# Optimization experiments

Hardware: AMD Instinct MI355X
Metric: run time of the kernel (lower is better)

## Reference

```python
import jax, jax.numpy as jnp
import numpy as np

B, S, IN, OUT, RANK, LORA_R = 2, 2048, 4096, 4096, 8, 16
LORA_SCALING = 16.0 / LORA_R  # alpha / r = 1.0


def setup_inputs() -> dict:
    key = jax.random.key(0)
    ks = jax.random.split(key, 6)
    x = jax.random.normal(ks[0], (B, S, IN), dtype=jnp.float32)
    weight = jax.random.normal(ks[1], (OUT, IN), dtype=jnp.float32) * 0.02  # Q (snapped weights)
    scale_A = jax.random.normal(ks[2], (OUT, RANK), dtype=jnp.float32) * 0.1
    scale_B = jax.random.normal(ks[3], (RANK, IN), dtype=jnp.float32) * 0.1
    rank_magnitude = jnp.ones((RANK,), dtype=jnp.float32)
    lora_A = jax.random.normal(ks[4], (LORA_R, IN), dtype=jnp.float32) * 0.02
    lora_B = jax.random.normal(ks[5], (OUT, LORA_R), dtype=jnp.float32) * 0.02
    return {"x": x, "weight": weight, "scale_A": scale_A, "scale_B": scale_B,
            "rank_magnitude": rank_magnitude, "lora_A": lora_A, "lora_B": lora_B}


def reference(x, weight, scale_A, scale_B, rank_magnitude, lora_A, lora_B):
    # y_o = sum_k g_k * a_{ok} * sum_i Q_{oi} * b_{ki} * x_i
    #     = sum_i (Q_{oi} * sum_k (g_k a_{ok}) b_{ki}) x_i
    # i.e. a single dense GEMM with the precomputed effective weight
    # W_eff = Q * ((scale_A * g) @ scale_B)  -- same math, rank dim folded once.
    S_mat = jnp.einsum('ok,ki->oi', scale_A * rank_magnitude[None, :], scale_B)  # [out, in]
    W_eff = weight * S_mat                                                        # [out, in]
    y = jnp.einsum('bsi,oi->bso', x, W_eff)                                       # [B, S, out]
    # LoRA add: (x @ A^T) @ B^T * scaling
    y = y + ((x @ lora_A.T) @ lora_B.T) * LORA_SCALING
    return y
```

## Files before the change

kernel.cpp:

```cpp
#include <hip/hip_runtime.h>

#define M_DIM 4096
#define IN_DIM 4096
#define OUT_DIM 4096
#define RANK 8
#define LORA_R 16
#define LORA_SCALING 1.0f

typedef __bf16 bf16;
typedef bf16  bf16x4 __attribute__((ext_vector_type(4)));
typedef bf16  bf16x8 __attribute__((ext_vector_type(8)));
typedef float f32x4  __attribute__((ext_vector_type(4)));
typedef float f32x16 __attribute__((ext_vector_type(16)));

#define OG 8
__global__ __launch_bounds__(256) void prep_weight(
    const float* __restrict__ weight, const float* __restrict__ scale_A,
    const float* __restrict__ scale_B, const float* __restrict__ g,
    const float* __restrict__ lora_A, const float* __restrict__ lora_B,
    bf16* __restrict__ wt)
{
    __shared__ float s_sa[OG][RANK];
    __shared__ float s_lb[OG][LORA_R];
    const int o0 = blockIdx.x * OG;
    const int t  = threadIdx.x;
    if (t < OG * RANK) {
        int r8 = t / RANK, k = t % RANK;
        s_sa[r8][k] = scale_A[(o0 + r8) * RANK + k] * g[k];
    }
    if (t < OG * LORA_R) {
        int r8 = t / LORA_R, r = t % LORA_R;
        s_lb[r8][r] = lora_B[(o0 + r8) * LORA_R + r] * LORA_SCALING;
    }
    __syncthreads();

    const int i0 = (blockIdx.y * 256 + t) * 4;

    f32x4 acc[OG];
#pragma unroll
    for (int r8 = 0; r8 < OG; ++r8) acc[r8] = {0.f, 0.f, 0.f, 0.f};
#pragma unroll
    for (int k = 0; k < RANK; ++k) {
        f32x4 sbk = *(const f32x4*)(scale_B + k * IN_DIM + i0);
#pragma unroll
        for (int r8 = 0; r8 < OG; ++r8) acc[r8] += s_sa[r8][k] * sbk;
    }
#pragma unroll
    for (int r8 = 0; r8 < OG; ++r8) {
        f32x4 wv = *(const f32x4*)(weight + (size_t)(o0 + r8) * IN_DIM + i0);
        acc[r8] *= wv;
    }
#pragma unroll
    for (int r = 0; r < LORA_R; ++r) {
        f32x4 lak = *(const f32x4*)(lora_A + r * IN_DIM + i0);
#pragma unroll
        for (int r8 = 0; r8 < OG; ++r8) acc[r8] += s_lb[r8][r] * lak;
    }
#pragma unroll
    for (int r8 = 0; r8 < OG; ++r8) {
        bf16x4 h = { (bf16)acc[r8][0], (bf16)acc[r8][1],
                     (bf16)acc[r8][2], (bf16)acc[r8][3] };
        *(bf16x4*)(wt + (size_t)(o0 + r8) * IN_DIM + i0) = h;
    }
}

__global__ __launch_bounds__(256) void cast_x(
    const float* __restrict__ x, bf16* __restrict__ xb, int n4)
{
    int idx    = blockIdx.x * blockDim.x + threadIdx.x;
    int stride = gridDim.x * blockDim.x;
    for (int i = idx; i < n4; i += stride) {
        f32x4 v = *(const f32x4*)(x + (size_t)i * 4);
        bf16x4 h = { (bf16)v[0], (bf16)v[1], (bf16)v[2], (bf16)v[3] };
        *(bf16x4*)(xb + (size_t)i * 4) = h;
    }
}

#define BM 128
#define BN 128
#define BK 32

__device__ __forceinline__ void gload_lds16(const bf16* g, bf16* l) {
    __builtin_amdgcn_global_load_lds(
        (const __attribute__((address_space(1))) void*)g,
        (__attribute__((address_space(3))) void*)l,
        16, 0, 0);
}

__global__ __launch_bounds__(256) void gemm_bt(
    const bf16* __restrict__ A,
    const bf16* __restrict__ Bw,
    float* __restrict__ C)
{
    __shared__ __align__(16) char smem[16896];
    bf16* sA = (bf16*)smem;
    bf16* sB = (bf16*)(smem + 8192);

    const int t    = threadIdx.x;
    const int w    = t >> 6;
    const int lane = t & 63;
    const int lh   = lane >> 5;
    const int ln   = lane & 31;

    const int bid = blockIdx.x;
    const int xcd = bid & 7;
    const int rr_ = bid >> 3;
    const int m0  = (xcd * 4 + (rr_ & 3)) * BM;
    const int n0  = (rr_ >> 2) * BN;

    const int wm = (w >> 1) * 64;
    const int wn = (w & 1) * 64;

    const int srow = t >> 2;
    const int scol = ((t & 3) ^ (srow & 3)) * 8;
    const bf16* gA0 = A  + (size_t)(m0 + srow)      * IN_DIM + scol;
    const bf16* gA1 = A  + (size_t)(m0 + 64 + srow) * IN_DIM + scol;
    const bf16* gB0 = Bw + (size_t)(n0 + srow)      * IN_DIM + scol;
    const bf16* gB1 = Bw + (size_t)(n0 + 64 + srow) * IN_DIM + scol;
    bf16* lA0 = sA + w * 512;
    bf16* lA1 = sA + 2048 + w * 512;
    bf16* lB0 = sB + w * 512;
    bf16* lB1 = sB + 2048 + w * 512;

    const bf16* pA[2][2];
    const bf16* pB[2][2];
#pragma unroll
    for (int tm = 0; tm < 2; ++tm) {
        int rowA = wm + tm * 32 + ln;
        int rowB = wn + tm * 32 + ln;
#pragma unroll
        for (int s = 0; s < 2; ++s) {
            pA[tm][s] = sA + rowA * 32 + (((s * 2 + lh) ^ (rowA & 3)) * 8);
            pB[tm][s] = sB + rowB * 32 + (((s * 2 + lh) ^ (rowB & 3)) * 8);
        }
    }

    f32x16 acc[2][2] = {};

    for (int k0 = 0; k0 < IN_DIM; k0 += BK) {
        __syncthreads();
        gload_lds16(gA0 + k0, lA0);
        gload_lds16(gA1 + k0, lA1);
        gload_lds16(gB0 + k0, lB0);
        gload_lds16(gB1 + k0, lB1);
        __syncthreads();

        bf16x8 af[2][2], bf_[2][2];
#pragma unroll
        for (int tm = 0; tm < 2; ++tm)
#pragma unroll
            for (int s = 0; s < 2; ++s) {
                af[tm][s]  = *(const bf16x8*)pA[tm][s];
                bf_[tm][s] = *(const bf16x8*)pB[tm][s];
            }
#pragma unroll
        for (int s = 0; s < 2; ++s)
#pragma unroll
            for (int tm = 0; tm < 2; ++tm)
#pragma unroll
                for (int tn = 0; tn < 2; ++tn)
                    acc[tm][tn] = __builtin_amdgcn_mfma_f32_32x32x16_bf16(
                        af[tm][s], bf_[tn][s], acc[tm][tn], 0, 0, 0);
    }

    __syncthreads();
    float* sEw = (float*)smem + w * (32 * 33);
#pragma unroll
    for (int tm = 0; tm < 2; ++tm)
#pragma unroll
        for (int tn = 0; tn < 2; ++tn) {
#pragma unroll
            for (int j = 0; j < 16; ++j) {
                int row = (j & 3) + 8 * (j >> 2) + 4 * lh;
                sEw[row * 33 + ln] = acc[tm][tn][j];
            }
#pragma unroll
            for (int p = 0; p < 4; ++p) {
                int r4 = p * 8 + (lane >> 3);
                int c4 = (lane & 7) * 4;
                f32x4 v = { sEw[r4 * 33 + c4],     sEw[r4 * 33 + c4 + 1],
                            sEw[r4 * 33 + c4 + 2], sEw[r4 * 33 + c4 + 3] };
                *(f32x4*)(C + (size_t)(m0 + wm + tm * 32 + r4) * OUT_DIM
                            + (n0 + wn + tn * 32 + c4)) = v;
            }
        }
}

extern "C" void kernel_launch(void* const* d_in, const int* in_sizes, int n_in,
                              void* d_out, int out_size, void* d_ws, size_t ws_size,
                              hipStream_t stream) {
    (void)in_sizes; (void)n_in; (void)out_size; (void)ws_size;
    const float* x        = (const float*)d_in[0];
    const float* weight   = (const float*)d_in[1];
    const float* scale_A  = (const float*)d_in[2];
    const float* scale_B  = (const float*)d_in[3];
    const float* g        = (const float*)d_in[4];
    const float* lora_A   = (const float*)d_in[5];
    const float* lora_B   = (const float*)d_in[6];
    float* out = (float*)d_out;

    bf16* xb = (bf16*)d_ws;
    bf16* wt = (bf16*)((char*)d_ws + (size_t)M_DIM * IN_DIM * sizeof(bf16));

    dim3 pgrid(OUT_DIM / OG, IN_DIM / (256 * 4));
    prep_weight<<<pgrid, 256, 0, stream>>>(weight, scale_A, scale_B, g,
                                           lora_A, lora_B, wt);
    cast_x<<<2048, 256, 0, stream>>>(x, xb, (M_DIM * IN_DIM) / 4);

    gemm_bt<<<(M_DIM / BM) * (OUT_DIM / BN), 256, 0, stream>>>(xb, wt, out);
}
```

Baseline: 360.4 us.

## Fuse weight prep and x cast into one launch; change LDS swizzle pattern

Merges the weight-prep and x-cast kernels into a single launch, with the first 2048 blocks building the effective bf16 weight and the rest casting x. This removes one kernel launch and lets both memory-bound passes run concurrently. The GEMM's LDS XOR swizzle now keys on (row>>1)&3 instead of row&3, to cut bank conflicts on the MFMA fragment reads. The load-side and read-side swizzles must stay consistent; the load side uses (t>>3)&3, which equals (srow>>1)&3.

```diff
diff --git a/kernel.cpp b/kernel.cpp
--- a/kernel.cpp
+++ b/kernel.cpp
@@ -14,65 +14,64 @@
 typedef float f32x16 __attribute__((ext_vector_type(16)));
 
 #define OG 8
-__global__ __launch_bounds__(256) void prep_weight(
+__global__ __launch_bounds__(256) void prep_fused(
     const float* __restrict__ weight, const float* __restrict__ scale_A,
     const float* __restrict__ scale_B, const float* __restrict__ g,
     const float* __restrict__ lora_A, const float* __restrict__ lora_B,
-    bf16* __restrict__ wt)
+    const float* __restrict__ x, bf16* __restrict__ wt, bf16* __restrict__ xb)
 {
-    __shared__ float s_sa[OG][RANK];
-    __shared__ float s_lb[OG][LORA_R];
-    const int o0 = blockIdx.x * OG;
-    const int t  = threadIdx.x;
-    if (t < OG * RANK) {
-        int r8 = t / RANK, k = t % RANK;
-        s_sa[r8][k] = scale_A[(o0 + r8) * RANK + k] * g[k];
-    }
-    if (t < OG * LORA_R) {
-        int r8 = t / LORA_R, r = t % LORA_R;
-        s_lb[r8][r] = lora_B[(o0 + r8) * LORA_R + r] * LORA_SCALING;
-    }
-    __syncthreads();
-
-    const int i0 = (blockIdx.y * 256 + t) * 4;
-
-    f32x4 acc[OG];
-#pragma unroll
-    for (int r8 = 0; r8 < OG; ++r8) acc[r8] = {0.f, 0.f, 0.f, 0.f};
-#pragma unroll
-    for (int k = 0; k < RANK; ++k) {
-        f32x4 sbk = *(const f32x4*)(scale_B + k * IN_DIM + i0);
-#pragma unroll
-        for (int r8 = 0; r8 < OG; ++r8) acc[r8] += s_sa[r8][k] * sbk;
-    }
-#pragma unroll
-    for (int r8 = 0; r8 < OG; ++r8) {
-        f32x4 wv = *(const f32x4*)(weight + (size_t)(o0 + r8) * IN_DIM + i0);
-        acc[r8] *= wv;
-    }
-#pragma unroll
-    for (int r = 0; r < LORA_R; ++r) {
-        f32x4 lak = *(const f32x4*)(lora_A + r * IN_DIM + i0);
-#pragma unroll
-        for (int r8 = 0; r8 < OG; ++r8) acc[r8] += s_lb[r8][r] * lak;
-    }
-#pragma unroll
-    for (int r8 = 0; r8 < OG; ++r8) {
-        bf16x4 h = { (bf16)acc[r8][0], (bf16)acc[r8][1],
-                     (bf16)acc[r8][2], (bf16)acc[r8][3] };
-        *(bf16x4*)(wt + (size_t)(o0 + r8) * IN_DIM + i0) = h;
-    }
-}
-
-__global__ __launch_bounds__(256) void cast_x(
-    const float* __restrict__ x, bf16* __restrict__ xb, int n4)
-{
-    int idx    = blockIdx.x * blockDim.x + threadIdx.x;
-    int stride = gridDim.x * blockDim.x;
-    for (int i = idx; i < n4; i += stride) {
-        f32x4 v = *(const f32x4*)(x + (size_t)i * 4);
-        bf16x4 h = { (bf16)v[0], (bf16)v[1], (bf16)v[2], (bf16)v[3] };
-        *(bf16x4*)(xb + (size_t)i * 4) = h;
+    const int t = threadIdx.x;
+    if (blockIdx.x < 2048) {
+        __shared__ float s_sa[OG][RANK];
+        __shared__ float s_lb[OG][LORA_R];
+        const int o0 = (blockIdx.x >> 2) * OG;
+        if (t < OG * RANK) {
+            int r8 = t / RANK, k = t % RANK;
+            s_sa[r8][k] = scale_A[(o0 + r8) * RANK + k] * g[k];
+        }
+        if (t < OG * LORA_R) {
+            int r8 = t / LORA_R, r = t % LORA_R;
+            s_lb[r8][r] = lora_B[(o0 + r8) * LORA_R + r] * LORA_SCALING;
+        }
+        __syncthreads();
+
+        const int i0 = ((blockIdx.x & 3) * 256 + t) * 4;
+
+        f32x4 acc[OG];
+#pragma unroll
+        for (int r8 = 0; r8 < OG; ++r8) acc[r8] = {0.f, 0.f, 0.f, 0.f};
+#pragma unroll
+        for (int k = 0; k < RANK; ++k) {
+            f32x4 sbk = *(const f32x4*)(scale_B + k * IN_DIM + i0);
+#pragma unroll
+            for (int r8 = 0; r8 < OG; ++r8) acc[r8] += s_sa[r8][k] * sbk;
+        }
+#pragma unroll
+        for (int r8 = 0; r8 < OG; ++r8) {
+            f32x4 wv = *(const f32x4*)(weight + (size_t)(o0 + r8) * IN_DIM + i0);
+            acc[r8] *= wv;
+        }
+#pragma unroll
+        for (int r = 0; r < LORA_R; ++r) {
+            f32x4 lak = *(const f32x4*)(lora_A + r * IN_DIM + i0);
+#pragma unroll
+            for (int r8 = 0; r8 < OG; ++r8) acc[r8] += s_lb[r8][r] * lak;
+        }
+#pragma unroll
+        for (int r8 = 0; r8 < OG; ++r8) {
+            bf16x4 h = { (bf16)acc[r8][0], (bf16)acc[r8][1],
+                         (bf16)acc[r8][2], (bf16)acc[r8][3] };
+            *(bf16x4*)(wt + (size_t)(o0 + r8) * IN_DIM + i0) = h;
+        }
+    } else {
+        const int n4  = (M_DIM * IN_DIM) / 4;
+        int idx    = (blockIdx.x - 2048) * 256 + t;
+        int stride = 2048 * 256;
+        for (int i = idx; i < n4; i += stride) {
+            f32x4 v = *(const f32x4*)(x + (size_t)i * 4);
+            bf16x4 h = { (bf16)v[0], (bf16)v[1], (bf16)v[2], (bf16)v[3] };
+            *(bf16x4*)(xb + (size_t)i * 4) = h;
+        }
     }
 }
 
@@ -112,7 +111,7 @@
     const int wn = (w & 1) * 64;
 
     const int srow = t >> 2;
-    const int scol = ((t & 3) ^ (srow & 3)) * 8;
+    const int scol = ((t & 3) ^ ((t >> 3) & 3)) * 8;
     const bf16* gA0 = A  + (size_t)(m0 + srow)      * IN_DIM + scol;
     const bf16* gA1 = A  + (size_t)(m0 + 64 + srow) * IN_DIM + scol;
     const bf16* gB0 = Bw + (size_t)(n0 + srow)      * IN_DIM + scol;
@@ -130,8 +129,8 @@
         int rowB = wn + tm * 32 + ln;
 #pragma unroll
         for (int s = 0; s < 2; ++s) {
-            pA[tm][s] = sA + rowA * 32 + (((s * 2 + lh) ^ (rowA & 3)) * 8);
-            pB[tm][s] = sB + rowB * 32 + (((s * 2 + lh) ^ (rowB & 3)) * 8);
+            pA[tm][s] = sA + rowA * 32 + (((s * 2 + lh) ^ ((rowA >> 1) & 3)) * 8);
+            pB[tm][s] = sB + rowB * 32 + (((s * 2 + lh) ^ ((rowB >> 1) & 3)) * 8);
         }
     }
 
@@ -202,10 +201,8 @@
     bf16* xb = (bf16*)d_ws;
     bf16* wt = (bf16*)((char*)d_ws + (size_t)M_DIM * IN_DIM * sizeof(bf16));
 
-    dim3 pgrid(OUT_DIM / OG, IN_DIM / (256 * 4));
-    prep_weight<<<pgrid, 256, 0, stream>>>(weight, scale_A, scale_B, g,
-                                           lora_A, lora_B, wt);
-    cast_x<<<2048, 256, 0, stream>>>(x, xb, (M_DIM * IN_DIM) / 4);
+    prep_fused<<<4096, 256, 0, stream>>>(weight, scale_A, scale_B, g,
+                                         lora_A, lora_B, x, wt, xb);
 
     gemm_bt<<<(M_DIM / BM) * (OUT_DIM / BN), 256, 0, stream>>>(xb, wt, out);
 }
```

New measurement: 338.1 us. 1.07x faster.
